# Kernel tuning notes

Hardware: AMD Instinct MI355X
Metric: run time of the kernel (lower is better)

## Reference

```python
import jax, jax.numpy as jnp
import numpy as np

D_MODEL = 256
NHEAD = 8
HEAD_DIM = D_MODEL // NHEAD
EPS_ATTN = 1e-6
EPS_LN = 1e-5


def _layernorm(x, g, b):
    mu = jnp.mean(x, axis=-1, keepdims=True)
    var = jnp.mean(jnp.square(x - mu), axis=-1, keepdims=True)
    return (x - mu) * jax.lax.rsqrt(var + EPS_LN) * g + b


def _embed_rotary(t, cos, sin):
    # t, cos, sin: [N, L, C]; interleaved pair rotation as in RoFPE.embed_rotary
    t2 = jnp.stack([-t[..., 1::2], t[..., ::2]], axis=-1).reshape(t.shape)
    return t * cos + t2 * sin


def setup_inputs() -> dict:
    key = jax.random.key(0)
    ks = jax.random.split(key, 12)
    N, L, S, C = 4, 4800, 4800, D_MODEL
    w = lambda k, shp: jax.random.normal(k, shp, dtype=jnp.float32) * 0.05
    return {
        "x": jax.random.normal(ks[0], (N, L, C), dtype=jnp.float32),
        "source": jax.random.normal(ks[1], (N, S, C), dtype=jnp.float32),
        "x_pe": jax.random.normal(ks[2], (N, L, C, 2), dtype=jnp.float32),
        "source_pe": jax.random.normal(ks[3], (N, S, C, 2), dtype=jnp.float32),
        "Wq": w(ks[4], (C, C)),
        "Wk": w(ks[5], (C, C)),
        "Wv": w(ks[6], (C, C)),
        "Wm": w(ks[7], (C, C)),
        "W1": w(ks[8], (2 * C, 2 * C)),
        "W2": w(ks[9], (C, 2 * C)),
        "g1": jnp.ones((C,), dtype=jnp.float32),
        "b1": jnp.zeros((C,), dtype=jnp.float32),
        "g2": jnp.ones((C,), dtype=jnp.float32),
        "b2": jnp.zeros((C,), dtype=jnp.float32),
    }


def reference(x, source, x_pe, source_pe, Wq, Wk, Wv, Wm, W1, W2, g1, b1, g2, b2):
    bs, L, C = x.shape
    H, D = NHEAD, HEAD_DIM
    # projections (nn.Linear: y = x @ W.T)
    q = x @ Wq.T
    k = source @ Wk.T
    v = source @ Wv.T
    # inline rotary PE
    q = _embed_rotary(q, x_pe[..., 0], x_pe[..., 1]).reshape(bs, L, H, D)
    k = _embed_rotary(k, source_pe[..., 0], source_pe[..., 1]).reshape(bs, -1, H, D)
    v = v.reshape(bs, -1, H, D)
    # LoFTR linear attention: phi(x) = elu(x) + 1
    Q = jax.nn.elu(q) + 1.0
    K = jax.nn.elu(k) + 1.0
    v_len = v.shape[1]
    vals = v / v_len
    KV = jnp.einsum("nshd,nshv->nhdv", K, vals)          # [N,H,D,D]
    Z = 1.0 / (jnp.einsum("nlhd,nhd->nlh", Q, K.sum(axis=1)) + EPS_ATTN)
    msg = jnp.einsum("nlhd,nhdv,nlh->nlhv", Q, KV, Z) * v_len  # [N,L,H,D]
    # merge + norm1
    msg = msg.reshape(bs, L, H * D) @ Wm.T
    msg = _layernorm(msg, g1, b1)
    # concat-MLP + norm2 + residual
    h = jnp.concatenate([x, msg], axis=-1)               # [N,L,2C]
    h = jax.nn.relu(h @ W1.T) @ W2.T
    h = _layernorm(h, g2, b2)
    return x + h
```

## Files before the change

### kernel.cpp

```cpp
#include <hip/hip_runtime.h>
#include <hip/hip_bf16.h>
#include <math.h>

#define NROWS 19200
#define SLEN  4800
#define KV_CHUNKS 50
#define KV_SC     96

typedef unsigned short ushort_t;
typedef __attribute__((ext_vector_type(8))) short bf16x8;
typedef __attribute__((ext_vector_type(4))) float f32x4;
typedef __attribute__((ext_vector_type(8))) unsigned short ushort8;

__device__ __forceinline__ float bf2f(ushort_t u) {
  union { unsigned int i; float f; } x; x.i = ((unsigned int)u) << 16; return x.f;
}
__device__ __forceinline__ ushort_t f2bf(float f) {
  __hip_bfloat16 h = __float2bfloat16(f);
  union { __hip_bfloat16 h; ushort_t u; } x; x.h = h; return x.u;
}

#define GLOAD16(g, l) __builtin_amdgcn_global_load_lds( \
    (const __attribute__((address_space(1))) unsigned int*)(g), \
    (__attribute__((address_space(3))) unsigned int*)(l), 16, 0, 0)

template <int EPI, bool CONCAT>
__device__ __forceinline__ void gemmT_body(
    const ushort_t* __restrict__ A0, const ushort_t* __restrict__ A1,
    const ushort_t* __restrict__ W, ushort_t* __restrict__ outp,
    int Nn, int K, int bm, int bn, char* smem) {
  const int tid = threadIdx.x;
  const int wave = tid >> 6, lane = tid & 63;
  const int wm = (wave >> 1) * 64, wn = (wave & 1) * 64;
  const int l15 = lane & 15, l4 = lane >> 4;

  f32x4 acc[4][4];
#pragma unroll
  for (int i = 0; i < 4; ++i)
#pragma unroll
    for (int j = 0; j < 4; ++j) acc[i][j] = (f32x4){0.f, 0.f, 0.f, 0.f};

  for (int k0 = 0; k0 < K; k0 += 64) {
    const ushort_t* Asrc;
    int ka;
    if (CONCAT) { Asrc = (k0 < 256) ? A0 : A1; ka = k0 & 255; }
    else        { Asrc = A0; ka = k0; }
#pragma unroll
    for (int c = 0; c < 4; ++c) {
      int ch = c * 4 + wave;
      int o = ch * 1024 + lane * 16;
      int row = o >> 7, g = (o >> 4) & 7;
      const ushort_t* sp =
          Asrc + (size_t)(bm + row) * 256 + ka + ((g ^ (row & 7)) << 3);
      GLOAD16(sp, smem + ch * 1024);
    }
#pragma unroll
    for (int c = 0; c < 4; ++c) {
      int ch = c * 4 + wave;
      int o = ch * 1024 + lane * 16;
      int row = o >> 7, g = (o >> 4) & 7;
      const ushort_t* sp =
          W + (size_t)(bn + row) * K + k0 + ((g ^ (row & 7)) << 3);
      GLOAD16(sp, smem + 16384 + ch * 1024);
    }
    __syncthreads();
#pragma unroll
    for (int kc = 0; kc < 2; ++kc) {
      bf16x8 af[4], bfr[4];
#pragma unroll
      for (int mi = 0; mi < 4; ++mi) {
        int r = wm + mi * 16 + l15;
        int G = kc * 4 + l4;
        af[mi] = *(const bf16x8*)(smem + r * 128 + ((G ^ (r & 7)) << 4));
      }
#pragma unroll
      for (int ni = 0; ni < 4; ++ni) {
        int r = wn + ni * 16 + l15;
        int G = kc * 4 + l4;
        bfr[ni] = *(const bf16x8*)(smem + 16384 + r * 128 +
                                   ((G ^ (r & 7)) << 4));
      }
#pragma unroll
      for (int mi = 0; mi < 4; ++mi)
#pragma unroll
        for (int ni = 0; ni < 4; ++ni)
          acc[mi][ni] = __builtin_amdgcn_mfma_f32_16x16x32_bf16(
              af[mi], bfr[ni], acc[mi][ni], 0, 0, 0);
    }
    __syncthreads();
  }

  ushort_t* st = (ushort_t*)smem;
#pragma unroll
  for (int mi = 0; mi < 4; ++mi)
#pragma unroll
    for (int ni = 0; ni < 4; ++ni)
#pragma unroll
      for (int j = 0; j < 4; ++j) {
        int trow = wm + mi * 16 + l4 * 4 + j;
        int tcol = wn + ni * 16 + l15;
        float v = acc[mi][ni][j];
        if (EPI == 3) v = fmaxf(v, 0.f);
        st[trow * 140 + tcol] = f2bf(v);
      }
  __syncthreads();
#pragma unroll
  for (int c = 0; c < 8; ++c) {
    int ch = c * 256 + tid;
    int row = ch >> 4, g = ch & 15;
    ushort8 u = *(const ushort8*)&st[row * 140 + g * 8];
    *(ushort8*)&outp[(size_t)(bm + row) * Nn + bn + g * 8] = u;
  }
}

__global__ __launch_bounds__(256) void qkv_fused(
    const ushort_t* __restrict__ xb, const ushort_t* __restrict__ srcb,
    const ushort_t* __restrict__ Wqb, const ushort_t* __restrict__ Wkb,
    const ushort_t* __restrict__ Wvb,
    ushort_t* __restrict__ Q, ushort_t* __restrict__ Kb,
    ushort_t* __restrict__ Vb) {
  extern __shared__ char smem[];
  int b = blockIdx.x;
  const int which = b < 300 ? 0 : (b < 600 ? 1 : 2);
  b -= which * 300;
  const int bm = (b >> 1) * 128, bn = (b & 1) * 128;
  const ushort_t* A = (which == 0) ? xb : srcb;
  const ushort_t* W = (which == 0) ? Wqb : (which == 1 ? Wkb : Wvb);
  ushort_t* o = (which == 0) ? Q : (which == 1 ? Kb : Vb);
  gemmT_body<0, false>(A, nullptr, W, o, 256, 256, bm, bn, smem);
}

__global__ __launch_bounds__(256) void mlp1_kernel(
    const ushort_t* __restrict__ xb, const ushort_t* __restrict__ msgln,
    const ushort_t* __restrict__ W1b, ushort_t* __restrict__ h1) {
  extern __shared__ char smem[];
  const int bm = (blockIdx.x >> 2) * 128, bn = (blockIdx.x & 3) * 128;
  gemmT_body<3, true>(xb, msgln, W1b, h1, 512, 512, bm, bn, smem);
}

__global__ __launch_bounds__(256) void msg_merge_ln(
    const ushort_t* __restrict__ Qb, const float* __restrict__ x_pe,
    const float* __restrict__ KVt, const float* __restrict__ Ksum,
    const ushort_t* __restrict__ Wm,
    const float* __restrict__ g, const float* __restrict__ bb,
    ushort_t* __restrict__ msgln) {
  __shared__ ushort_t AsM[16 * 256];
  __shared__ ushort_t U[256 * 64];
  __shared__ float Ks[8][32];
  __shared__ float zS[16][8];
  __shared__ float partS[4][16];
  __shared__ float partQ[4][16];
  __shared__ float gS[256], bS[256];

  const int tid = threadIdx.x;
  const int wave = tid >> 6, lane = tid & 63;
  const int l15 = lane & 15, l4 = lane >> 4;
  const int bm = blockIdx.x * 16;
  const int n = bm / SLEN;

  gS[tid] = g[tid];
  bS[tid] = bb[tid];
  Ks[tid >> 5][tid & 31] = Ksum[(n * 8 + (tid >> 5)) * 32 + (tid & 31)];

  ushort_t* KVl = U;
#pragma unroll
  for (int c = 0; c < 8; ++c) {
    int e4 = c * 256 + tid;
    const float4 kv4 = *(const float4*)&KVt[(size_t)(n * 8) * 1024 + e4 * 4];
    int E = e4 * 4;
    int h = E >> 10, v = (E >> 5) & 31, d0 = E & 31;
    int gsw = (d0 >> 3) ^ ((v >> 1) & 3);
    ushort4 u = make_ushort4(f2bf(kv4.x), f2bf(kv4.y), f2bf(kv4.z),
                             f2bf(kv4.w));
    *(ushort4*)&KVl[h * 1024 + v * 32 + gsw * 8 + (d0 & 7)] = u;
  }

#pragma unroll
  for (int p = 0; p < 2; ++p) {
    int rr = p * 8 + (tid >> 5), cc = (tid & 31) * 8;
    const size_t eoff = (size_t)(bm + rr) * 256 + cc;
    const ushort8 uq = *(const ushort8*)&Qb[eoff];
    const float4* pp = (const float4*)&x_pe[eoff * 2];
    float4 p0 = pp[0], p1 = pp[1], p2 = pp[2], p3 = pp[3];
    float v[8];
#pragma unroll
    for (int i = 0; i < 8; ++i) v[i] = bf2f((ushort_t)uq[i]);
    float r[8];
    r[0] = v[0] * p0.x - v[1] * p0.y; r[1] = v[1] * p0.z + v[0] * p0.w;
    r[2] = v[2] * p1.x - v[3] * p1.y; r[3] = v[3] * p1.z + v[2] * p1.w;
    r[4] = v[4] * p2.x - v[5] * p2.y; r[5] = v[5] * p2.z + v[4] * p2.w;
    r[6] = v[6] * p3.x - v[7] * p3.y; r[7] = v[7] * p3.z + v[6] * p3.w;
    float w[8];
    ushort8 pk;
#pragma unroll
    for (int i = 0; i < 8; ++i) {
      w[i] = r[i] > 0.f ? r[i] + 1.f : __expf(r[i]);
      pk[i] = f2bf(w[i]);
    }
    int gi = cc >> 3;
    int gis = (gi & ~7) | ((gi & 7) ^ (rr & 7));
    *(ushort8*)&AsM[rr * 256 + gis * 8] = pk;
    const int hh = (tid & 31) >> 2;
    const int db = (tid & 3) * 8;
    float zp = 0.f;
#pragma unroll
    for (int i = 0; i < 8; ++i) zp += w[i] * Ks[hh][db + i];
    zp += __shfl_xor(zp, 1);
    zp += __shfl_xor(zp, 2);
    if ((tid & 3) == 0) zS[rr][hh] = 1.0f / (zp + 1e-6f);
  }
  __syncthreads();

  f32x4 macc[2][2];
#pragma unroll
  for (int hh2 = 0; hh2 < 2; ++hh2) {
    const int h = wave * 2 + hh2;
    bf16x8 af, bfr[2];
    {
      int r = l15;
      int gi = h * 4 + l4;
      int gis = (gi & ~7) | ((gi & 7) ^ (r & 7));
      af = *(const bf16x8*)&AsM[r * 256 + gis * 8];
    }
#pragma unroll
    for (int ni = 0; ni < 2; ++ni) {
      int v = ni * 16 + l15;
      int gsw = l4 ^ ((v >> 1) & 3);
      bfr[ni] = *(const bf16x8*)&KVl[h * 1024 + v * 32 + gsw * 8];
    }
#pragma unroll
    for (int ni = 0; ni < 2; ++ni)
      macc[hh2][ni] = __builtin_amdgcn_mfma_f32_16x16x32_bf16(
          af, bfr[ni], (f32x4){0.f, 0.f, 0.f, 0.f}, 0, 0, 0);
  }
  __syncthreads();

#pragma unroll
  for (int hh2 = 0; hh2 < 2; ++hh2) {
    const int h = wave * 2 + hh2;
#pragma unroll
    for (int ni = 0; ni < 2; ++ni)
#pragma unroll
      for (int j = 0; j < 4; ++j) {
        int row = l4 * 4 + j;
        int col = h * 32 + ni * 16 + l15;
        float mv = macc[hh2][ni][j] * zS[row][h];
        int gi = col >> 3;
        int gis = (gi & ~7) | ((gi & 7) ^ (row & 7));
        AsM[row * 256 + gis * 8 + (col & 7)] = f2bf(mv);
      }
  }

  ushort_t* Bs = U;
  f32x4 acc[4];
#pragma unroll
  for (int j = 0; j < 4; ++j) acc[j] = (f32x4){0.f, 0.f, 0.f, 0.f};

  for (int k0 = 0; k0 < 256; k0 += 64) {
#pragma unroll
    for (int c = 0; c < 8; ++c) {
      int ch = c * 256 + tid;
      int row = ch >> 3, gch = ch & 7;
      const ushort_t* src =
          Wm + (size_t)row * 256 + k0 + ((gch ^ (row & 7)) << 3);
      GLOAD16(src, (char*)Bs + ch * 16);
    }
    __syncthreads();
#pragma unroll
    for (int kc = 0; kc < 2; ++kc) {
      bf16x8 af, bfr[4];
      {
        int r = l15;
        int gi = (k0 >> 3) + kc * 4 + l4;
        int gis = (gi & ~7) | ((gi & 7) ^ (r & 7));
        af = *(const bf16x8*)&AsM[r * 256 + gis * 8];
      }
#pragma unroll
      for (int ni = 0; ni < 4; ++ni) {
        int r = wave * 64 + ni * 16 + l15;
        int G = kc * 4 + l4;
        bfr[ni] = *(const bf16x8*)((char*)Bs + r * 128 + ((G ^ (r & 7)) << 4));
      }
#pragma unroll
      for (int ni = 0; ni < 4; ++ni)
        acc[ni] = __builtin_amdgcn_mfma_f32_16x16x32_bf16(
            af, bfr[ni], acc[ni], 0, 0, 0);
    }
    __syncthreads();
  }

#pragma unroll
  for (int j = 0; j < 4; ++j) {
    float s = acc[0][j] + acc[1][j] + acc[2][j] + acc[3][j];
    float q = acc[0][j] * acc[0][j] + acc[1][j] * acc[1][j] +
              acc[2][j] * acc[2][j] + acc[3][j] * acc[3][j];
#pragma unroll
    for (int m = 1; m < 16; m <<= 1) {
      s += __shfl_xor(s, m);
      q += __shfl_xor(q, m);
    }
    if (l15 == 0) {
      int row = l4 * 4 + j;
      partS[wave][row] = s;
      partQ[wave][row] = q;
    }
  }
  __syncthreads();

  float mu[4], rsv[4];
#pragma unroll
  for (int j = 0; j < 4; ++j) {
    int row = l4 * 4 + j;
    float s = partS[0][row] + partS[1][row] + partS[2][row] + partS[3][row];
    float q2 = partQ[0][row] + partQ[1][row] + partQ[2][row] + partQ[3][row];
    float m_ = s * (1.f / 256.f);
    float var = q2 * (1.f / 256.f) - m_ * m_;
    mu[j] = m_;
    rsv[j] = rsqrtf(var + 1e-5f);
  }

#pragma unroll
  for (int ni = 0; ni < 4; ++ni)
#pragma unroll
    for (int j = 0; j < 4; ++j) {
      int row = l4 * 4 + j;
      int col2 = wave * 64 + ni * 16 + l15;
      float vv = (acc[ni][j] - mu[j]) * rsv[j] * gS[col2] + bS[col2];
      msgln[(size_t)(bm + row) * 256 + col2] = f2bf(vv);
    }
}

template <int KDIM, bool RESID, bool OUTBF>
__global__ __launch_bounds__(256) void gemm_ln_kernel(
    const ushort_t* __restrict__ A, const ushort_t* __restrict__ W,
    const float* __restrict__ g, const float* __restrict__ bb,
    const float* __restrict__ resid, void* __restrict__ outp) {
  __shared__ char As[32 * 128];
  __shared__ char Bs[256 * 128];
  __shared__ float partS[4][32];
  __shared__ float partQ[4][32];
  __shared__ float gS[256], bS[256];

  const int tid = threadIdx.x;
  const int wave = tid >> 6, lane = tid & 63;
  const int l15 = lane & 15, l4 = lane >> 4;
  const int bm = blockIdx.x * 32;

  gS[tid] = g[tid];
  bS[tid] = bb[tid];

  f32x4 acc[2][4];
#pragma unroll
  for (int i = 0; i < 2; ++i)
#pragma unroll
    for (int j = 0; j < 4; ++j) acc[i][j] = (f32x4){0.f, 0.f, 0.f, 0.f};

  for (int k0 = 0; k0 < KDIM; k0 += 64) {
    {
      int row = tid >> 3, gch = tid & 7;
      const ushort_t* src =
          A + (size_t)(bm + row) * KDIM + k0 + ((gch ^ (row & 7)) << 3);
      GLOAD16(src, As + tid * 16);
    }
#pragma unroll
    for (int c = 0; c < 8; ++c) {
      int ch = c * 256 + tid;
      int row = ch >> 3, gch = ch & 7;
      const ushort_t* src =
          W + (size_t)row * KDIM + k0 + ((gch ^ (row & 7)) << 3);
      GLOAD16(src, Bs + ch * 16);
    }
    __syncthreads();
#pragma unroll
    for (int kc = 0; kc < 2; ++kc) {
      bf16x8 af[2], bfr[4];
#pragma unroll
      for (int mi = 0; mi < 2; ++mi) {
        int r = mi * 16 + l15;
        int G = kc * 4 + l4;
        af[mi] = *(const bf16x8*)(As + r * 128 + ((G ^ (r & 7)) << 4));
      }
#pragma unroll
      for (int ni = 0; ni < 4; ++ni) {
        int r = wave * 64 + ni * 16 + l15;
        int G = kc * 4 + l4;
        bfr[ni] = *(const bf16x8*)(Bs + r * 128 + ((G ^ (r & 7)) << 4));
      }
#pragma unroll
      for (int mi = 0; mi < 2; ++mi)
#pragma unroll
        for (int ni = 0; ni < 4; ++ni)
          acc[mi][ni] = __builtin_amdgcn_mfma_f32_16x16x32_bf16(
              af[mi], bfr[ni], acc[mi][ni], 0, 0, 0);
    }
    __syncthreads();
  }

#pragma unroll
  for (int mi = 0; mi < 2; ++mi)
#pragma unroll
    for (int j = 0; j < 4; ++j) {
      float s = acc[mi][0][j] + acc[mi][1][j] + acc[mi][2][j] + acc[mi][3][j];
      float q = acc[mi][0][j] * acc[mi][0][j] + acc[mi][1][j] * acc[mi][1][j] +
                acc[mi][2][j] * acc[mi][2][j] + acc[mi][3][j] * acc[mi][3][j];
#pragma unroll
      for (int m = 1; m < 16; m <<= 1) {
        s += __shfl_xor(s, m);
        q += __shfl_xor(q, m);
      }
      if (l15 == 0) {
        int row = mi * 16 + l4 * 4 + j;
        partS[wave][row] = s;
        partQ[wave][row] = q;
      }
    }
  __syncthreads();

  float mu[2][4], rsv[2][4];
#pragma unroll
  for (int mi = 0; mi < 2; ++mi)
#pragma unroll
    for (int j = 0; j < 4; ++j) {
      int row = mi * 16 + l4 * 4 + j;
      float s = partS[0][row] + partS[1][row] + partS[2][row] + partS[3][row];
      float q2 = partQ[0][row] + partQ[1][row] + partQ[2][row] + partQ[3][row];
      float m_ = s * (1.f / 256.f);
      float var = q2 * (1.f / 256.f) - m_ * m_;
      mu[mi][j] = m_;
      rsv[mi][j] = rsqrtf(var + 1e-5f);
    }

#pragma unroll
  for (int mi = 0; mi < 2; ++mi)
#pragma unroll
    for (int ni = 0; ni < 4; ++ni)
#pragma unroll
      for (int j = 0; j < 4; ++j) {
        int row = mi * 16 + l4 * 4 + j;
        int col = wave * 64 + ni * 16 + l15;
        float v = (acc[mi][ni][j] - mu[mi][j]) * rsv[mi][j] * gS[col] + bS[col];
        size_t gr = (size_t)(bm + row);
        if (RESID) v += resid[gr * 256 + col];
        if (OUTBF)
          ((ushort_t*)outp)[gr * 256 + col] = f2bf(v);
        else
          ((float*)outp)[gr * 256 + col] = v;
      }
}

__global__ __launch_bounds__(256) void kv_partial(
    const ushort_t* __restrict__ Kb, const ushort_t* __restrict__ Vb,
    const float* __restrict__ s_pe,
    float* __restrict__ kvp, float* __restrict__ ksp) {
  __shared__ float bufK[32][32];
  __shared__ float bufV[32][32];
  const int b = blockIdx.x;
  const int ch = b % KV_CHUNKS;
  const int nh = b / KV_CHUNKS;
  const int h = nh & 7, n = nh >> 3;
  const int tid = threadIdx.x;
  const int d = tid >> 3, vb = (tid & 7) * 4;
  const int half = tid >> 7, t = tid & 127;
  const int srow = t >> 2, seg = (t & 3) * 8;
  const int segS = (seg + 8 * (srow & 3)) & 31;
  float a0 = 0.f, a1 = 0.f, a2 = 0.f, a3 = 0.f, ks = 0.f;
  const size_t base = (size_t)n * SLEN * 256 + (size_t)h * 32;
  const int s0 = ch * KV_SC;
  for (int s = s0; s < s0 + KV_SC; s += 32) {
    __syncthreads();
    const size_t eoff = base + (size_t)(s + srow) * 256 + seg;
    ushort8 u = *(const ushort8*)((half ? Vb : Kb) + eoff);
    float v[8];
#pragma unroll
    for (int i = 0; i < 8; ++i) v[i] = bf2f((ushort_t)u[i]);
    if (!half) {
      const float4* pp = (const float4*)&s_pe[eoff * 2];
      float4 p0 = pp[0], p1 = pp[1], p2 = pp[2], p3 = pp[3];
      float r[8];
      r[0] = v[0] * p0.x - v[1] * p0.y; r[1] = v[1] * p0.z + v[0] * p0.w;
      r[2] = v[2] * p1.x - v[3] * p1.y; r[3] = v[3] * p1.z + v[2] * p1.w;
      r[4] = v[4] * p2.x - v[5] * p2.y; r[5] = v[5] * p2.z + v[4] * p2.w;
      r[6] = v[6] * p3.x - v[7] * p3.y; r[7] = v[7] * p3.z + v[6] * p3.w;
#pragma unroll
      for (int i = 0; i < 8; ++i)
        v[i] = r[i] > 0.f ? r[i] + 1.f : __expf(r[i]);
    }
    float* dst = half ? &bufV[srow][segS] : &bufK[srow][segS];
    *(float4*)dst = (float4){v[0], v[1], v[2], v[3]};
    *(float4*)(dst + 4) = (float4){v[4], v[5], v[6], v[7]};
    __syncthreads();
#pragma unroll
    for (int ss = 0; ss < 32; ++ss) {
      int rot = 8 * (ss & 3);
      float kd = bufK[ss][(d + rot) & 31];
      float4 vv = *(const float4*)&bufV[ss][(vb + rot) & 31];
      a0 += kd * vv.x; a1 += kd * vv.y; a2 += kd * vv.z; a3 += kd * vv.w;
      ks += kd;
    }
  }
  float* kv = &kvp[(size_t)b * 1024 + d * 32 + vb];
  kv[0] = a0; kv[1] = a1; kv[2] = a2; kv[3] = a3;
  if ((tid & 7) == 0) ksp[(size_t)b * 32 + d] = ks;
}

__global__ __launch_bounds__(256) void kv_reduce(
    const float* __restrict__ kvp, const float* __restrict__ ksp,
    float* __restrict__ KVt, float* __restrict__ Ksum) {
  const int nh = blockIdx.x;
  const int tid = threadIdx.x;
  for (int e = tid; e < 1024; e += 256) {
    float s = 0.f;
    for (int p = 0; p < KV_CHUNKS; ++p)
      s += kvp[(size_t)(nh * KV_CHUNKS + p) * 1024 + e];
    KVt[(size_t)nh * 1024 + (e & 31) * 32 + (e >> 5)] = s;
  }
  if (tid < 32) {
    float s = 0.f;
    for (int p = 0; p < KV_CHUNKS; ++p)
      s += ksp[(size_t)(nh * KV_CHUNKS + p) * 32 + tid];
    Ksum[nh * 32 + tid] = s;
  }
}

__global__ __launch_bounds__(256) void conv_all(
    const float* __restrict__ x, const float* __restrict__ src,
    const float* w0, const float* w1, const float* w2, const float* w3,
    const float* w4, const float* w5,
    ushort_t* __restrict__ xo, ushort_t* __restrict__ so,
    ushort_t* o0, ushort_t* o1, ushort_t* o2, ushort_t* o3, ushort_t* o4,
    ushort_t* o5) {
  int blk = blockIdx.x;
  if (blk < 4800) {
    const float* s; ushort_t* d;
    if (blk < 2400) { s = x; d = xo; } else { s = src; d = so; blk -= 2400; }
    size_t o = ((size_t)blk * 256 + threadIdx.x) * 8;
    float4 v0 = *(const float4*)&s[o];
    float4 v1 = *(const float4*)&s[o + 4];
    ushort8 u = {f2bf(v0.x), f2bf(v0.y), f2bf(v0.z), f2bf(v0.w),
                 f2bf(v1.x), f2bf(v1.y), f2bf(v1.z), f2bf(v1.w)};
    *(ushort8*)&d[o] = u;
  } else {
    int e = ((blk - 4800) * 256 + threadIdx.x) * 4;
    const float* s; ushort_t* d; int off;
    if      (e < 65536)  { s = w0; d = o0; off = e; }
    else if (e < 131072) { s = w1; d = o1; off = e - 65536; }
    else if (e < 196608) { s = w2; d = o2; off = e - 131072; }
    else if (e < 262144) { s = w3; d = o3; off = e - 196608; }
    else if (e < 524288) { s = w4; d = o4; off = e - 262144; }
    else                 { s = w5; d = o5; off = e - 524288; }
    float4 v = *(const float4*)&s[off];
    ushort4 u = make_ushort4(f2bf(v.x), f2bf(v.y), f2bf(v.z), f2bf(v.w));
    *(ushort4*)&d[off] = u;
  }
}

extern "C" void kernel_launch(void* const* d_in, const int* in_sizes, int n_in,
                              void* d_out, int out_size, void* d_ws,
                              size_t ws_size, hipStream_t stream) {
  const float* x    = (const float*)d_in[0];
  const float* src  = (const float*)d_in[1];
  const float* x_pe = (const float*)d_in[2];
  const float* s_pe = (const float*)d_in[3];
  const float* Wq = (const float*)d_in[4];
  const float* Wk = (const float*)d_in[5];
  const float* Wv = (const float*)d_in[6];
  const float* Wm = (const float*)d_in[7];
  const float* W1 = (const float*)d_in[8];
  const float* W2 = (const float*)d_in[9];
  const float* g1 = (const float*)d_in[10];
  const float* b1 = (const float*)d_in[11];
  const float* g2 = (const float*)d_in[12];
  const float* b2 = (const float*)d_in[13];
  float* out = (float*)d_out;

  const size_t R = (size_t)NROWS * 256;
  ushort_t* xb    = (ushort_t*)d_ws;
  ushort_t* srcb  = xb + R;
  ushort_t* Qb    = srcb + R;
  ushort_t* Kb    = Qb + R;
  ushort_t* Vb    = Kb + R;
  ushort_t* msgln = Vb + R;
  ushort_t* Wqb   = msgln + R;
  ushort_t* Wkb   = Wqb + 65536;
  ushort_t* Wvb   = Wkb + 65536;
  ushort_t* Wmb   = Wvb + 65536;
  ushort_t* W1b   = Wmb + 65536;
  ushort_t* W2b   = W1b + 262144;
  float* kvp      = (float*)(W2b + 131072);
  float* ksp      = kvp + 1638400;
  float* KVt      = ksp + 51200;
  float* Ksum     = KVt + 32768;
  ushort_t* h1   = Kb;

  dim3 blk(256);
  conv_all<<<5440, blk, 0, stream>>>(x, src, Wq, Wk, Wv, Wm, W1, W2,
                                     xb, srcb, Wqb, Wkb, Wvb, Wmb, W1b, W2b);
  qkv_fused<<<900, blk, 35840, stream>>>(xb, srcb, Wqb, Wkb, Wvb, Qb, Kb, Vb);
  kv_partial<<<1600, blk, 0, stream>>>(Kb, Vb, s_pe, kvp, ksp);
  kv_reduce<<<32, blk, 0, stream>>>(kvp, ksp, KVt, Ksum);
  msg_merge_ln<<<1200, blk, 0, stream>>>(Qb, x_pe, KVt, Ksum, Wmb, g1, b1,
                                         msgln);
  mlp1_kernel<<<600, blk, 35840, stream>>>(xb, msgln, W1b, h1);
  gemm_ln_kernel<512, true, false><<<600, blk, 0, stream>>>(
      h1, W2b, g2, b2, x, out);
}
```

Measured before the change: 118.7 us.

## Double-buffer GEMM tile loads and store reduced KV in bf16

The GEMM bodies (qkv, mlp1, gemm_ln) now use two LDS buffers, so the global-to-LDS loads for the next K tile are issued before computing on the current one. Each iteration ends with one explicit vmcnt wait plus barrier. kv_reduce writes KV in bf16, and msg_merge_ln loads it straight into LDS with global_load_lds instead of converting fp32 in registers. The cost is double the LDS use (64KB dynamic, about 73KB static in gemm_ln), which lowers occupancy.

Result: slower. 128.4 us (+8.1%).

```diff
diff --git a/kernel.cpp b/kernel.cpp
--- a/kernel.cpp
+++ b/kernel.cpp
@@ -23,6 +23,13 @@
 #define GLOAD16(g, l) __builtin_amdgcn_global_load_lds( \
     (const __attribute__((address_space(1))) unsigned int*)(g), \
     (__attribute__((address_space(3))) unsigned int*)(l), 16, 0, 0)
+
+__device__ __forceinline__ void pipe_barrier() {
+  asm volatile("s_waitcnt vmcnt(0)" ::: "memory");
+  __builtin_amdgcn_sched_barrier(0);
+  __builtin_amdgcn_s_barrier();
+  __builtin_amdgcn_sched_barrier(0);
+}
 
 template <int EPI, bool CONCAT>
 __device__ __forceinline__ void gemmT_body(
@@ -40,7 +47,7 @@
 #pragma unroll
     for (int j = 0; j < 4; ++j) acc[i][j] = (f32x4){0.f, 0.f, 0.f, 0.f};
 
-  for (int k0 = 0; k0 < K; k0 += 64) {
+  auto stage = [&](int buf, int k0) {
     const ushort_t* Asrc;
     int ka;
     if (CONCAT) { Asrc = (k0 < 256) ? A0 : A1; ka = k0 & 255; }
@@ -50,20 +57,28 @@
       int ch = c * 4 + wave;
       int o = ch * 1024 + lane * 16;
       int row = o >> 7, g = (o >> 4) & 7;
-      const ushort_t* sp =
-          Asrc + (size_t)(bm + row) * 256 + ka + ((g ^ (row & 7)) << 3);
-      GLOAD16(sp, smem + ch * 1024);
+      GLOAD16(Asrc + (size_t)(bm + row) * 256 + ka + ((g ^ (row & 7)) << 3),
+              smem + buf * 16384 + ch * 1024);
     }
 #pragma unroll
     for (int c = 0; c < 4; ++c) {
       int ch = c * 4 + wave;
       int o = ch * 1024 + lane * 16;
       int row = o >> 7, g = (o >> 4) & 7;
-      const ushort_t* sp =
-          W + (size_t)(bn + row) * K + k0 + ((g ^ (row & 7)) << 3);
-      GLOAD16(sp, smem + 16384 + ch * 1024);
-    }
-    __syncthreads();
+      GLOAD16(W + (size_t)(bn + row) * K + k0 + ((g ^ (row & 7)) << 3),
+              smem + 32768 + buf * 16384 + ch * 1024);
+    }
+  };
+
+  stage(0, 0);
+  pipe_barrier();
+
+  const int nT = K >> 6;
+  for (int t = 0; t < nT; ++t) {
+    const int cur = t & 1;
+    if (t + 1 < nT) stage(cur ^ 1, (t + 1) << 6);
+    const char* Ab = smem + cur * 16384;
+    const char* Bb = smem + 32768 + cur * 16384;
 #pragma unroll
     for (int kc = 0; kc < 2; ++kc) {
       bf16x8 af[4], bfr[4];
@@ -71,14 +86,13 @@
       for (int mi = 0; mi < 4; ++mi) {
         int r = wm + mi * 16 + l15;
         int G = kc * 4 + l4;
-        af[mi] = *(const bf16x8*)(smem + r * 128 + ((G ^ (r & 7)) << 4));
+        af[mi] = *(const bf16x8*)(Ab + r * 128 + ((G ^ (r & 7)) << 4));
       }
 #pragma unroll
       for (int ni = 0; ni < 4; ++ni) {
         int r = wn + ni * 16 + l15;
         int G = kc * 4 + l4;
-        bfr[ni] = *(const bf16x8*)(smem + 16384 + r * 128 +
-                                   ((G ^ (r & 7)) << 4));
+        bfr[ni] = *(const bf16x8*)(Bb + r * 128 + ((G ^ (r & 7)) << 4));
       }
 #pragma unroll
       for (int mi = 0; mi < 4; ++mi)
@@ -87,7 +101,7 @@
           acc[mi][ni] = __builtin_amdgcn_mfma_f32_16x16x32_bf16(
               af[mi], bfr[ni], acc[mi][ni], 0, 0, 0);
     }
-    __syncthreads();
+    pipe_barrier();
   }
 
   ushort_t* st = (ushort_t*)smem;
@@ -140,7 +154,7 @@
 
 __global__ __launch_bounds__(256) void msg_merge_ln(
     const ushort_t* __restrict__ Qb, const float* __restrict__ x_pe,
-    const float* __restrict__ KVt, const float* __restrict__ Ksum,
+    const ushort_t* __restrict__ KVtb, const float* __restrict__ Ksum,
     const ushort_t* __restrict__ Wm,
     const float* __restrict__ g, const float* __restrict__ bb,
     ushort_t* __restrict__ msgln) {
@@ -161,18 +175,17 @@
   gS[tid] = g[tid];
   bS[tid] = bb[tid];
   Ks[tid >> 5][tid & 31] = Ksum[(n * 8 + (tid >> 5)) * 32 + (tid & 31)];
+  __syncthreads();
 
   ushort_t* KVl = U;
 #pragma unroll
-  for (int c = 0; c < 8; ++c) {
-    int e4 = c * 256 + tid;
-    const float4 kv4 = *(const float4*)&KVt[(size_t)(n * 8) * 1024 + e4 * 4];
-    int E = e4 * 4;
-    int h = E >> 10, v = (E >> 5) & 31, d0 = E & 31;
-    int gsw = (d0 >> 3) ^ ((v >> 1) & 3);
-    ushort4 u = make_ushort4(f2bf(kv4.x), f2bf(kv4.y), f2bf(kv4.z),
-                             f2bf(kv4.w));
-    *(ushort4*)&KVl[h * 1024 + v * 32 + gsw * 8 + (d0 & 7)] = u;
+  for (int c = 0; c < 4; ++c) {
+    int ch = c * 256 + tid;
+    int e = ch * 8;
+    int h = e >> 10, v = (e >> 5) & 31, gd = (e >> 3) & 3;
+    int gsw = gd ^ ((v >> 1) & 3);
+    GLOAD16(KVtb + (size_t)(n * 8) * 1024 + h * 1024 + v * 32 + gsw * 8,
+            (char*)KVl + ch * 16);
   }
 
 #pragma unroll
@@ -335,8 +348,8 @@
     const ushort_t* __restrict__ A, const ushort_t* __restrict__ W,
     const float* __restrict__ g, const float* __restrict__ bb,
     const float* __restrict__ resid, void* __restrict__ outp) {
-  __shared__ char As[32 * 128];
-  __shared__ char Bs[256 * 128];
+  __shared__ char As[2][4096];
+  __shared__ char Bs[2][32768];
   __shared__ float partS[4][32];
   __shared__ float partQ[4][32];
   __shared__ float gS[256], bS[256];
@@ -355,22 +368,28 @@
 #pragma unroll
     for (int j = 0; j < 4; ++j) acc[i][j] = (f32x4){0.f, 0.f, 0.f, 0.f};
 
-  for (int k0 = 0; k0 < KDIM; k0 += 64) {
+  auto stage = [&](int buf, int k0) {
     {
       int row = tid >> 3, gch = tid & 7;
-      const ushort_t* src =
-          A + (size_t)(bm + row) * KDIM + k0 + ((gch ^ (row & 7)) << 3);
-      GLOAD16(src, As + tid * 16);
+      GLOAD16(A + (size_t)(bm + row) * KDIM + k0 + ((gch ^ (row & 7)) << 3),
+              As[buf] + tid * 16);
     }
 #pragma unroll
     for (int c = 0; c < 8; ++c) {
       int ch = c * 256 + tid;
       int row = ch >> 3, gch = ch & 7;
-      const ushort_t* src =
-          W + (size_t)row * KDIM + k0 + ((gch ^ (row & 7)) << 3);
-      GLOAD16(src, Bs + ch * 16);
-    }
-    __syncthreads();
+      GLOAD16(W + (size_t)row * KDIM + k0 + ((gch ^ (row & 7)) << 3),
+              Bs[buf] + ch * 16);
+    }
+  };
+
+  stage(0, 0);
+  pipe_barrier();
+
+  const int nT = KDIM >> 6;
+  for (int t = 0; t < nT; ++t) {
+    const int cur = t & 1;
+    if (t + 1 < nT) stage(cur ^ 1, (t + 1) << 6);
 #pragma unroll
     for (int kc = 0; kc < 2; ++kc) {
       bf16x8 af[2], bfr[4];
@@ -378,13 +397,13 @@
       for (int mi = 0; mi < 2; ++mi) {
         int r = mi * 16 + l15;
         int G = kc * 4 + l4;
-        af[mi] = *(const bf16x8*)(As + r * 128 + ((G ^ (r & 7)) << 4));
+        af[mi] = *(const bf16x8*)(As[cur] + r * 128 + ((G ^ (r & 7)) << 4));
       }
 #pragma unroll
       for (int ni = 0; ni < 4; ++ni) {
         int r = wave * 64 + ni * 16 + l15;
         int G = kc * 4 + l4;
-        bfr[ni] = *(const bf16x8*)(Bs + r * 128 + ((G ^ (r & 7)) << 4));
+        bfr[ni] = *(const bf16x8*)(Bs[cur] + r * 128 + ((G ^ (r & 7)) << 4));
       }
 #pragma unroll
       for (int mi = 0; mi < 2; ++mi)
@@ -393,7 +412,7 @@
           acc[mi][ni] = __builtin_amdgcn_mfma_f32_16x16x32_bf16(
               af[mi], bfr[ni], acc[mi][ni], 0, 0, 0);
     }
-    __syncthreads();
+    pipe_barrier();
   }
 
 #pragma unroll
@@ -505,14 +524,14 @@
 
 __global__ __launch_bounds__(256) void kv_reduce(
     const float* __restrict__ kvp, const float* __restrict__ ksp,
-    float* __restrict__ KVt, float* __restrict__ Ksum) {
+    ushort_t* __restrict__ KVtb, float* __restrict__ Ksum) {
   const int nh = blockIdx.x;
   const int tid = threadIdx.x;
   for (int e = tid; e < 1024; e += 256) {
     float s = 0.f;
     for (int p = 0; p < KV_CHUNKS; ++p)
       s += kvp[(size_t)(nh * KV_CHUNKS + p) * 1024 + e];
-    KVt[(size_t)nh * 1024 + (e & 31) * 32 + (e >> 5)] = s;
+    KVtb[(size_t)nh * 1024 + (e & 31) * 32 + (e >> 5)] = f2bf(s);
   }
   if (tid < 32) {
     float s = 0.f;
@@ -588,19 +607,19 @@
   ushort_t* W2b   = W1b + 262144;
   float* kvp      = (float*)(W2b + 131072);
   float* ksp      = kvp + 1638400;
-  float* KVt      = ksp + 51200;
-  float* Ksum     = KVt + 32768;
+  ushort_t* KVtb  = (ushort_t*)(ksp + 51200);
+  float* Ksum     = (float*)(KVtb + 32768);
   ushort_t* h1   = Kb;
 
   dim3 blk(256);
   conv_all<<<5440, blk, 0, stream>>>(x, src, Wq, Wk, Wv, Wm, W1, W2,
                                      xb, srcb, Wqb, Wkb, Wvb, Wmb, W1b, W2b);
-  qkv_fused<<<900, blk, 35840, stream>>>(xb, srcb, Wqb, Wkb, Wvb, Qb, Kb, Vb);
+  qkv_fused<<<900, blk, 65536, stream>>>(xb, srcb, Wqb, Wkb, Wvb, Qb, Kb, Vb);
   kv_partial<<<1600, blk, 0, stream>>>(Kb, Vb, s_pe, kvp, ksp);
-  kv_reduce<<<32, blk, 0, stream>>>(kvp, ksp, KVt, Ksum);
-  msg_merge_ln<<<1200, blk, 0, stream>>>(Qb, x_pe, KVt, Ksum, Wmb, g1, b1,
+  kv_reduce<<<32, blk, 0, stream>>>(kvp, ksp, KVtb, Ksum);
+  msg_merge_ln<<<1200, blk, 0, stream>>>(Qb, x_pe, KVtb, Ksum, Wmb, g1, b1,
                                          msgln);
-  mlp1_kernel<<<600, blk, 35840, stream>>>(xb, msgln, W1b, h1);
+  mlp1_kernel<<<600, blk, 65536, stream>>>(xb, msgln, W1b, h1);
   gemm_ln_kernel<512, true, false><<<600, blk, 0, stream>>>(
       h1, W2b, g2, b2, x, out);
 }
```

## Fuse KV reduction into kv_partial via atomics and read bf16 residual

Applied to the files above, without the earlier changes.

Removes the separate kv_reduce kernel by having each kv_partial block atomically add its partial KV and K-sum into the final transposed buffers, which are zeroed by extra blocks appended to conv_all. The final GEMM+LN residual is now read from the bf16 copy of x instead of the fp32 input, halving that read traffic at some precision cost. A missing __syncthreads after the LDS KV staging in msg_merge_ln is also added. Atomics introduce contention on 32 KB of targets and nondeterministic summation order.

Result: no change. 117.4 us, median of 2 (-1.1%).

```diff
diff --git a/kernel.cpp b/kernel.cpp
--- a/kernel.cpp
+++ b/kernel.cpp
@@ -174,6 +174,7 @@
                              f2bf(kv4.w));
     *(ushort4*)&KVl[h * 1024 + v * 32 + gsw * 8 + (d0 & 7)] = u;
   }
+  __syncthreads();
 
 #pragma unroll
   for (int p = 0; p < 2; ++p) {
@@ -334,7 +335,7 @@
 __global__ __launch_bounds__(256) void gemm_ln_kernel(
     const ushort_t* __restrict__ A, const ushort_t* __restrict__ W,
     const float* __restrict__ g, const float* __restrict__ bb,
-    const float* __restrict__ resid, void* __restrict__ outp) {
+    const ushort_t* __restrict__ residb, void* __restrict__ outp) {
   __shared__ char As[32 * 128];
   __shared__ char Bs[256 * 128];
   __shared__ float partS[4][32];
@@ -440,7 +441,7 @@
         int col = wave * 64 + ni * 16 + l15;
         float v = (acc[mi][ni][j] - mu[mi][j]) * rsv[mi][j] * gS[col] + bS[col];
         size_t gr = (size_t)(bm + row);
-        if (RESID) v += resid[gr * 256 + col];
+        if (RESID) v += bf2f(residb[gr * 256 + col]);
         if (OUTBF)
           ((ushort_t*)outp)[gr * 256 + col] = f2bf(v);
         else
@@ -451,7 +452,7 @@
 __global__ __launch_bounds__(256) void kv_partial(
     const ushort_t* __restrict__ Kb, const ushort_t* __restrict__ Vb,
     const float* __restrict__ s_pe,
-    float* __restrict__ kvp, float* __restrict__ ksp) {
+    float* __restrict__ KVt, float* __restrict__ Ksum) {
   __shared__ float bufK[32][32];
   __shared__ float bufV[32][32];
   const int b = blockIdx.x;
@@ -498,28 +499,12 @@
       ks += kd;
     }
   }
-  float* kv = &kvp[(size_t)b * 1024 + d * 32 + vb];
-  kv[0] = a0; kv[1] = a1; kv[2] = a2; kv[3] = a3;
-  if ((tid & 7) == 0) ksp[(size_t)b * 32 + d] = ks;
-}
-
-__global__ __launch_bounds__(256) void kv_reduce(
-    const float* __restrict__ kvp, const float* __restrict__ ksp,
-    float* __restrict__ KVt, float* __restrict__ Ksum) {
-  const int nh = blockIdx.x;
-  const int tid = threadIdx.x;
-  for (int e = tid; e < 1024; e += 256) {
-    float s = 0.f;
-    for (int p = 0; p < KV_CHUNKS; ++p)
-      s += kvp[(size_t)(nh * KV_CHUNKS + p) * 1024 + e];
-    KVt[(size_t)nh * 1024 + (e & 31) * 32 + (e >> 5)] = s;
-  }
-  if (tid < 32) {
-    float s = 0.f;
-    for (int p = 0; p < KV_CHUNKS; ++p)
-      s += ksp[(size_t)(nh * KV_CHUNKS + p) * 32 + tid];
-    Ksum[nh * 32 + tid] = s;
-  }
+  float* kvh = &KVt[(size_t)nh * 1024 + d];
+  atomicAdd(kvh + (vb + 0) * 32, a0);
+  atomicAdd(kvh + (vb + 1) * 32, a1);
+  atomicAdd(kvh + (vb + 2) * 32, a2);
+  atomicAdd(kvh + (vb + 3) * 32, a3);
+  if ((tid & 7) == 0) atomicAdd(&Ksum[nh * 32 + d], ks);
 }
 
 __global__ __launch_bounds__(256) void conv_all(
@@ -528,7 +513,7 @@
     const float* w4, const float* w5,
     ushort_t* __restrict__ xo, ushort_t* __restrict__ so,
     ushort_t* o0, ushort_t* o1, ushort_t* o2, ushort_t* o3, ushort_t* o4,
-    ushort_t* o5) {
+    ushort_t* o5, float* __restrict__ kvz) {
   int blk = blockIdx.x;
   if (blk < 4800) {
     const float* s; ushort_t* d;
@@ -539,7 +524,7 @@
     ushort8 u = {f2bf(v0.x), f2bf(v0.y), f2bf(v0.z), f2bf(v0.w),
                  f2bf(v1.x), f2bf(v1.y), f2bf(v1.z), f2bf(v1.w)};
     *(ushort8*)&d[o] = u;
-  } else {
+  } else if (blk < 5440) {
     int e = ((blk - 4800) * 256 + threadIdx.x) * 4;
     const float* s; ushort_t* d; int off;
     if      (e < 65536)  { s = w0; d = o0; off = e; }
@@ -551,6 +536,9 @@
     float4 v = *(const float4*)&s[off];
     ushort4 u = make_ushort4(f2bf(v.x), f2bf(v.y), f2bf(v.z), f2bf(v.w));
     *(ushort4*)&d[off] = u;
+  } else {
+    int e = ((blk - 5440) * 256 + threadIdx.x) * 4;
+    *(float4*)&kvz[e] = (float4){0.f, 0.f, 0.f, 0.f};
   }
 }
 
@@ -586,21 +574,19 @@
   ushort_t* Wmb   = Wvb + 65536;
   ushort_t* W1b   = Wmb + 65536;
   ushort_t* W2b   = W1b + 262144;
-  float* kvp      = (float*)(W2b + 131072);
-  float* ksp      = kvp + 1638400;
-  float* KVt      = ksp + 51200;
+  float* KVt      = (float*)(W2b + 131072);
   float* Ksum     = KVt + 32768;
   ushort_t* h1   = Kb;
 
   dim3 blk(256);
-  conv_all<<<5440, blk, 0, stream>>>(x, src, Wq, Wk, Wv, Wm, W1, W2,
-                                     xb, srcb, Wqb, Wkb, Wvb, Wmb, W1b, W2b);
+  conv_all<<<5473, blk, 0, stream>>>(x, src, Wq, Wk, Wv, Wm, W1, W2,
+                                     xb, srcb, Wqb, Wkb, Wvb, Wmb, W1b, W2b,
+                                     KVt);
   qkv_fused<<<900, blk, 35840, stream>>>(xb, srcb, Wqb, Wkb, Wvb, Qb, Kb, Vb);
-  kv_partial<<<1600, blk, 0, stream>>>(Kb, Vb, s_pe, kvp, ksp);
-  kv_reduce<<<32, blk, 0, stream>>>(kvp, ksp, KVt, Ksum);
+  kv_partial<<<1600, blk, 0, stream>>>(Kb, Vb, s_pe, KVt, Ksum);
   msg_merge_ln<<<1200, blk, 0, stream>>>(Qb, x_pe, KVt, Ksum, Wmb, g1, b1,
                                          msgln);
   mlp1_kernel<<<600, blk, 35840, stream>>>(xb, msgln, W1b, h1);
   gemm_ln_kernel<512, true, false><<<600, blk, 0, stream>>>(
-      h1, W2b, g2, b2, x, out);
-}
+      h1, W2b, g2, b2, xb, out);
+}
```
